# Optimization experiments

Measured on AMD Instinct MI355X. Metric: run time of the kernel, lower is better.

## Reference

```python
import jax, jax.numpy as jnp
import numpy as np

EMBED = 1024
HEADS = 16
HEAD_DIM = EMBED // HEADS


def setup_inputs() -> dict:
    key = jax.random.key(0)
    ks = jax.random.split(key, 12)
    B, S = 2, 2048
    inp = {
        'v': jax.random.normal(ks[0], (B, S, EMBED), jnp.float32),
        'k': jax.random.normal(ks[1], (B, S, EMBED), jnp.float32),
        'q': jax.random.normal(ks[2], (B, S, EMBED), jnp.float32),
        'mask': jnp.ones((B, 1, S, S), dtype=bool),
        'Wv': jax.random.normal(ks[3], (EMBED, EMBED), jnp.float32) * 0.02,
        'bv': jax.random.normal(ks[4], (EMBED,), jnp.float32) * 0.02,
        'Wk': jax.random.normal(ks[5], (EMBED, EMBED), jnp.float32) * 0.02,
        'bk': jax.random.normal(ks[6], (EMBED,), jnp.float32) * 0.02,
        'Wq': jax.random.normal(ks[7], (EMBED, EMBED), jnp.float32) * 0.02,
        'bq': jax.random.normal(ks[8], (EMBED,), jnp.float32) * 0.02,
        'Wo': jax.random.normal(ks[9], (EMBED, EMBED), jnp.float32) * 0.02,
        'bo': jax.random.normal(ks[10], (EMBED,), jnp.float32) * 0.02,
    }
    return inp


def reference(v, k, q, mask, Wv, bv, Wk, bk, Wq, bq, Wo, bo):
    N, q_len, _ = q.shape
    k_len = k.shape[1]
    # linear projections (torch Linear: x @ W.T + b)
    vh = (v @ Wv.T + bv).reshape(N, -1, HEADS, HEAD_DIM)
    kh = (k @ Wk.T + bk).reshape(N, k_len, HEADS, HEAD_DIM)
    qh = (q @ Wq.T + bq).reshape(N, q_len, HEADS, HEAD_DIM)
    # scores [N, H, q, k]
    energy = jnp.einsum('nqhd,nkhd->nhqk', qh, kh)
    # NOTE: original masks BEFORE dividing by sqrt(embed_size)
    energy = jnp.where(mask, energy, jnp.float32(-1e20))
    attention = jax.nn.softmax(energy / jnp.sqrt(jnp.float32(EMBED)), axis=3)
    out = jnp.einsum('nhqk,nkhd->nqhd', attention, vh).reshape(N, q_len, EMBED)
    return out @ Wo.T + bo
```

## Files before the change

kernel.cpp:

```cpp
#include <hip/hip_runtime.h>
#include <cstdint>
#include <cstddef>


typedef uint16_t u16;
typedef uint32_t u32;
typedef unsigned long long u64;
using bf16x8 = __attribute__((ext_vector_type(8))) __bf16;
using bf16x2 = __attribute__((ext_vector_type(2))) __bf16;
using f32x4  = __attribute__((ext_vector_type(4))) float;
using f32x16 = __attribute__((ext_vector_type(16))) float;
using u16x8  = __attribute__((ext_vector_type(8))) uint16_t;
using u16x4  = __attribute__((ext_vector_type(4))) uint16_t;
using u32x4  = __attribute__((ext_vector_type(4))) uint32_t;

#define S_LEN 2048
#define EMB   1024
#define NHEAD 16
#define HDIM  64
#define BATCH 2
#define MROWS (BATCH * S_LEN)
#define NBITW (BATCH * S_LEN * (S_LEN / 64))

__device__ __forceinline__ u16 f2bf(float f) {
  uint32_t u = __float_as_uint(f);
  u += 0x7FFFu + ((u >> 16) & 1u);
  return (u16)(u >> 16);
}

__device__ __forceinline__ float fexp2(float x) {
#if __has_builtin(__builtin_amdgcn_exp2f)
  return __builtin_amdgcn_exp2f(x);
#else
  return exp2f(x);
#endif
}

__device__ __forceinline__ u32 packbf(float a, float b) {
  bf16x2 v = { (__bf16)a, (__bf16)b };
  return __builtin_bit_cast(u32, v);
}

__device__ __forceinline__ void plswap(u32& a, u32& b) {
  asm volatile("v_permlane32_swap_b32 %0, %1" : "+v"(a), "+v"(b));
}

__device__ __forceinline__ float xhalf_sum(float x) {
  u32 a = __builtin_bit_cast(u32, x), b;
  asm volatile("v_mov_b32 %0, %1" : "=v"(b) : "v"(a));
  asm volatile("v_permlane32_swap_b32 %0, %1" : "+v"(a), "+v"(b));
  return __builtin_bit_cast(float, a) + __builtin_bit_cast(float, b);
}

__device__ __forceinline__ float tree16(const f32x16& v) {
  float t0 = v[0] + v[1], t1 = v[2] + v[3], t2 = v[4] + v[5], t3 = v[6] + v[7];
  float t4 = v[8] + v[9], t5 = v[10] + v[11], t6 = v[12] + v[13], t7 = v[14] + v[15];
  float u0 = t0 + t1, u1 = t2 + t3, u2 = t4 + t5, u3 = t6 + t7;
  return (u0 + u1) + (u2 + u3);
}

__device__ __forceinline__ void async16(void* lds, const void* g) {
  __builtin_amdgcn_global_load_lds(
      (const __attribute__((address_space(1))) void*)g,
      (__attribute__((address_space(3))) void*)lds, 16, 0, 0);
}

__global__ __launch_bounds__(256) void mask_compact(const uint32_t* __restrict__ m,
                                                    u64* __restrict__ bits) {
  const int i = blockIdx.x * 256 + threadIdx.x;
  if (i >= NBITW) return;
  const bool bytew = (m[0] == 0x01010101u);
  u64 b = 0;
  if (bytew) {
    const uint32_t* src = m + (size_t)i * 16;
#pragma unroll
    for (int w = 0; w < 16; ++w) {
      const uint32_t v = src[w];
#pragma unroll
      for (int j = 0; j < 4; ++j)
        b |= (u64)(((v >> (8 * j)) & 0xFFu) != 0u) << (w * 4 + j);
    }
  } else {
    const uint32_t* src = m + (size_t)i * 64;
#pragma unroll
    for (int j = 0; j < 64; ++j) b |= (u64)(src[j] != 0u) << j;
  }
  bits[i] = b;
}

struct ConvArgs {
  const float* src[4];
  u16* dst[4];
};

__global__ __launch_bounds__(256) void convert_bf16(ConvArgs a) {
  const int j = blockIdx.y;
  const float4* s = (const float4*)a.src[j];
  u16* d = a.dst[j];
  const int n4 = EMB * EMB / 4;
  for (int i = blockIdx.x * 256 + threadIdx.x; i < n4; i += gridDim.x * 256) {
    float4 v = s[i];
    u16x4 o = { f2bf(v.x), f2bf(v.y), f2bf(v.z), f2bf(v.w) };
    *(u16x4*)(d + (size_t)i * 4) = o;
  }
}

__device__ __forceinline__ void gemm_fused_body(const float* __restrict__ A,
                                                const u16* __restrict__ W,
                                                const float* __restrict__ bias,
                                                u16* __restrict__ C, float scale) {
  constexpr int K = 1024, N = 1024;
  __shared__ alignas(16) u16 As[128 * 32];
  __shared__ alignas(16) u16 Bs[128 * 32];
  const int t = threadIdx.x;
  const int wave = t >> 6, lane = t & 63;
  const int wr = wave >> 1, wc = wave & 1;
  const int m0 = blockIdx.y * 128, n0 = blockIdx.x * 128;
  f32x4 acc[4][4] = {};
  const int srow = wave * 16 + (lane >> 2);
  const int soff = (lane & 3) * 8;
  const u16* gB = W + (size_t)(n0 + srow) * K + soff;
  u16* lB = Bs + wave * 512;
  const int ar = t >> 1, ah = t & 1;
  const float* ga = A + (size_t)(m0 + ar) * K + ah * 16;
  u16* aw = As + ar * 32 + ah * 16;
  const int fo = (lane >> 4) * 8;
  const int fr = lane & 15;

  float4 v0 = *(const float4*)(ga + 0);
  float4 v1 = *(const float4*)(ga + 4);
  float4 v2 = *(const float4*)(ga + 8);
  float4 v3 = *(const float4*)(ga + 12);

  for (int kt = 0; kt < K; kt += 32) {
    {
      u16x8 w0 = { f2bf(v0.x), f2bf(v0.y), f2bf(v0.z), f2bf(v0.w),
                   f2bf(v1.x), f2bf(v1.y), f2bf(v1.z), f2bf(v1.w) };
      u16x8 w1 = { f2bf(v2.x), f2bf(v2.y), f2bf(v2.z), f2bf(v2.w),
                   f2bf(v3.x), f2bf(v3.y), f2bf(v3.z), f2bf(v3.w) };
      *(u16x8*)aw = w0;
      *(u16x8*)(aw + 8) = w1;
    }
    async16(lB,        gB + kt);
    async16(lB + 2048, gB + (size_t)64 * K + kt);
    __syncthreads();
    bf16x8 af[4], bfr[4];
#pragma unroll
    for (int i = 0; i < 4; ++i)
      af[i] = *(const bf16x8*)(As + (wr * 64 + i * 16 + fr) * 32 + fo);
#pragma unroll
    for (int i = 0; i < 4; ++i)
      bfr[i] = *(const bf16x8*)(Bs + (wc * 64 + i * 16 + fr) * 32 + fo);
#pragma unroll
    for (int mi = 0; mi < 4; ++mi)
#pragma unroll
      for (int ni = 0; ni < 4; ++ni)
        acc[mi][ni] = __builtin_amdgcn_mfma_f32_16x16x32_bf16(af[mi], bfr[ni],
                                                              acc[mi][ni], 0, 0, 0);
    if (kt + 32 < K) {
      v0 = *(const float4*)(ga + kt + 32);
      v1 = *(const float4*)(ga + kt + 36);
      v2 = *(const float4*)(ga + kt + 40);
      v3 = *(const float4*)(ga + kt + 44);
    }
    __syncthreads();
  }
  const int r0 = (lane >> 4) * 4;
#pragma unroll
  for (int mi = 0; mi < 4; ++mi) {
    const int rowb = m0 + wr * 64 + mi * 16 + r0;
#pragma unroll
    for (int ni = 0; ni < 4; ++ni) {
      const int col = n0 + wc * 64 + ni * 16 + fr;
      const float bv = bias[col];
#pragma unroll
      for (int r = 0; r < 4; ++r)
        C[(size_t)(rowb + r) * N + col] = f2bf((acc[mi][ni][r] + bv) * scale);
    }
  }
}

struct ProjArgs {
  const float* A[3];
  const u16* W[3];
  const float* bias[3];
  u16* C[3];
  float scale[3];
};

__global__ __launch_bounds__(256) void gemm_proj3(ProjArgs p) {
  const int z = blockIdx.z;
  gemm_fused_body(p.A[z], p.W[z], p.bias[z], p.C[z], p.scale[z]);
}

__global__ __launch_bounds__(256) void gemm_out(const u16* __restrict__ A,
                                                const u16* __restrict__ W,
                                                const float* __restrict__ bias,
                                                float* __restrict__ C) {
  constexpr int BM = 64, BN = 128, FM = 2, FN = 4;
  constexpr int K = 1024, N = 1024;
  __shared__ alignas(16) u16 As[BM * 32];
  __shared__ alignas(16) u16 Bs[BN * 32];
  const int t = threadIdx.x;
  const int wave = t >> 6, lane = t & 63;
  const int wr = wave >> 1, wc = wave & 1;
  const int m0 = blockIdx.y * BM, n0 = blockIdx.x * BN;
  f32x4 acc[FM][FN] = {};
  const int srow = wave * 16 + (lane >> 2);
  const int soff = (lane & 3) * 8;
  const u16* gA = A + (size_t)(m0 + srow) * K + soff;
  const u16* gB = W + (size_t)(n0 + srow) * K + soff;
  u16* lA = As + wave * 512;
  u16* lB = Bs + wave * 512;
  const int fo = (lane >> 4) * 8;
  const int fr = lane & 15;

  for (int kt = 0; kt < K; kt += 32) {
    async16(lA, gA + kt);
#pragma unroll
    for (int a = 0; a < BN / 64; ++a)
      async16(lB + a * 2048, gB + (size_t)(a * 64) * K + kt);
    __syncthreads();
    bf16x8 af[FM], bfr[FN];
#pragma unroll
    for (int i = 0; i < FM; ++i)
      af[i] = *(const bf16x8*)(As + (wr * (FM * 16) + i * 16 + fr) * 32 + fo);
#pragma unroll
    for (int i = 0; i < FN; ++i)
      bfr[i] = *(const bf16x8*)(Bs + (wc * (FN * 16) + i * 16 + fr) * 32 + fo);
#pragma unroll
    for (int mi = 0; mi < FM; ++mi)
#pragma unroll
      for (int ni = 0; ni < FN; ++ni)
        acc[mi][ni] = __builtin_amdgcn_mfma_f32_16x16x32_bf16(af[mi], bfr[ni],
                                                              acc[mi][ni], 0, 0, 0);
    __syncthreads();
  }
  const int r0 = (lane >> 4) * 4;
#pragma unroll
  for (int mi = 0; mi < FM; ++mi) {
    const int rowb = m0 + wr * (FM * 16) + mi * 16 + r0;
#pragma unroll
    for (int ni = 0; ni < FN; ++ni) {
      const int col = n0 + wc * (FN * 16) + ni * 16 + fr;
      const float bv = bias[col];
#pragma unroll
      for (int r = 0; r < 4; ++r)
        C[(size_t)(rowb + r) * N + col] = acc[mi][ni][r] + bv;
    }
  }
}

__global__ __launch_bounds__(256, 2) void attn_fa(const u16* __restrict__ Qh,
                                                  const u16* __restrict__ Kh,
                                                  const u16* __restrict__ Vh,
                                                  const u64* __restrict__ mbits,
                                                  u16* __restrict__ O) {
  __shared__ alignas(16) u16 Kt[2][64 * 64];
  __shared__ alignas(16) u16 Vt[2][64 * 64];
  const int t = threadIdx.x, wave = t >> 6, lane = t & 63;
  const int lin = blockIdx.x + 16 * blockIdx.y;
  const int logical = (lin & 7) * 64 + (lin >> 3);
  const int wbx = logical & 15;
  const int wbh = logical >> 4;
  const int b = wbh >> 4, h = wbh & 15;
  const int ql = lane & 31;
  const int hi = lane >> 5;
  const int qrow = wbx * 128 + wave * 32 + ql;

  const u16* qbase = Qh + (size_t)(b * S_LEN + qrow) * EMB + h * HDIM + hi * 8;
  bf16x8 qf[4];
#pragma unroll
  for (int dk = 0; dk < 4; ++dk)
    qf[dk] = *(const bf16x8*)(qbase + dk * 16);

  const int srow = t >> 3;
  const int schunk = t & 7;
  const int fk0 = (srow + (srow >> 3)) & 7;
  const int fk1 = (srow + 32 + ((srow + 32) >> 3)) & 7;
  const u16* kbase = Kh + (size_t)(b * S_LEN) * EMB + h * HDIM;
  const u16* vbase = Vh + (size_t)(b * S_LEN) * EMB + h * HDIM;
  const int vdg = t & 7, vkp = t >> 3;
  const int vd0 = vdg * 8, vk0 = vkp * 2;
  const int vg_hi = (vkp >> 2) & 7, vg_lo = (vkp & 3) * 4;

  u16x8 va, vb;
  {
    async16(&Kt[0][0] + wave * 512,
            kbase + (size_t)srow * EMB + ((schunk ^ fk0) * 8));
    async16(&Kt[0][0] + 2048 + wave * 512,
            kbase + (size_t)(srow + 32) * EMB + ((schunk ^ fk1) * 8));
    const u16* vs = vbase + (size_t)vk0 * EMB + vd0;
    va = *(const u16x8*)vs;
    vb = *(const u16x8*)(vs + EMB);
  }
#pragma unroll
  for (int j = 0; j < 8; ++j) {
    const int d = vd0 + j;
    const int fd = (d + (d >> 3)) & 7;
    const u32 val = (u32)va[j] | ((u32)vb[j] << 16);
    *(u32*)((char*)&Vt[0][0] + (d * 128 + ((vg_hi ^ fd) << 4) + vg_lo)) = val;
  }
  __syncthreads();

  f32x16 o[2] = {};
  float lloc = 0.f;
  const u64* mword = mbits + (size_t)(b * S_LEN + qrow) * 32;

  for (int kt = 0; kt < 32; ++kt) {
    const int cur = kt & 1, nxt = cur ^ 1;
    if (kt < 31) {
      const int kvn = (kt + 1) * 64;
      async16(&Kt[nxt][0] + wave * 512,
              kbase + (size_t)(kvn + srow) * EMB + ((schunk ^ fk0) * 8));
      async16(&Kt[nxt][0] + 2048 + wave * 512,
              kbase + (size_t)(kvn + srow + 32) * EMB + ((schunk ^ fk1) * 8));
      const u16* vs = vbase + (size_t)(kvn + vk0) * EMB + vd0;
      va = *(const u16x8*)vs;
      vb = *(const u16x8*)(vs + EMB);
    }

    f32x16 s[2] = {};
    __builtin_amdgcn_s_setprio(1);
#pragma unroll
    for (int kb = 0; kb < 2; ++kb) {
      const int key = kb * 32 + ql;
      const int fkk = (key + (key >> 3)) & 7;
      const char* kRow = (const char*)&Kt[cur][0] + key * 128;
#pragma unroll
      for (int dk = 0; dk < 4; ++dk) {
        const bf16x8 kf =
            *(const bf16x8*)(kRow + (((dk * 2 + hi) ^ fkk) << 4));
        s[kb] = __builtin_amdgcn_mfma_f32_32x32x16_bf16(kf, qf[dk], s[kb], 0, 0, 0);
      }
    }
    __builtin_amdgcn_s_setprio(0);

    const u64 mw = mword[kt];
    if (!__all((int)(mw == ~0ull))) {
#pragma unroll
      for (int kb = 0; kb < 2; ++kb)
#pragma unroll
        for (int r = 0; r < 16; ++r) {
          const int key = 32 * kb + (r & 3) + 8 * (r >> 2) + 4 * hi;
          if (!((mw >> key) & 1ull)) s[kb][r] = -1.0e20f;
        }
    }

#pragma unroll
    for (int kb = 0; kb < 2; ++kb)
#pragma unroll
      for (int r = 0; r < 16; ++r) s[kb][r] = fexp2(s[kb][r]);
    lloc += tree16(s[0]) + tree16(s[1]);

    bf16x8 pf[4];
#pragma unroll
    for (int kb = 0; kb < 2; ++kb) {
      u32 w0 = packbf(s[kb][0], s[kb][1]);
      u32 w1 = packbf(s[kb][2], s[kb][3]);
      u32 w2 = packbf(s[kb][4], s[kb][5]);
      u32 w3 = packbf(s[kb][6], s[kb][7]);
      u32 w4 = packbf(s[kb][8], s[kb][9]);
      u32 w5 = packbf(s[kb][10], s[kb][11]);
      u32 w6 = packbf(s[kb][12], s[kb][13]);
      u32 w7 = packbf(s[kb][14], s[kb][15]);
      plswap(w0, w2);
      plswap(w1, w3);
      plswap(w4, w6);
      plswap(w5, w7);
      const u32x4 lo4 = {w0, w1, w2, w3};
      const u32x4 hi4 = {w4, w5, w6, w7};
      pf[kb * 2 + 0] = __builtin_bit_cast(bf16x8, lo4);
      pf[kb * 2 + 1] = __builtin_bit_cast(bf16x8, hi4);
    }

    __builtin_amdgcn_s_setprio(1);
#pragma unroll
    for (int dB = 0; dB < 2; ++dB) {
      const int d = dB * 32 + ql;
      const int fd = (d + (d >> 3)) & 7;
      const char* vRow = (const char*)&Vt[cur][0] + d * 128;
#pragma unroll
      for (int ks = 0; ks < 4; ++ks) {
        const bf16x8 vf =
            *(const bf16x8*)(vRow + (((ks * 2 + hi) ^ fd) << 4));
        o[dB] = __builtin_amdgcn_mfma_f32_32x32x16_bf16(vf, pf[ks], o[dB], 0, 0, 0);
      }
    }
    __builtin_amdgcn_s_setprio(0);

    if (kt < 31) {
#pragma unroll
      for (int j = 0; j < 8; ++j) {
        const int d = vd0 + j;
        const int fd = (d + (d >> 3)) & 7;
        const u32 val = (u32)va[j] | ((u32)vb[j] << 16);
        *(u32*)((char*)&Vt[nxt][0] + (d * 128 + ((vg_hi ^ fd) << 4) + vg_lo)) = val;
      }
    }
    __syncthreads();
  }

  const float inv = 1.0f / xhalf_sum(lloc);
  u16* ob = O + (size_t)(b * S_LEN + qrow) * EMB + h * HDIM;
#pragma unroll
  for (int dB = 0; dB < 2; ++dB)
#pragma unroll
    for (int rr = 0; rr < 4; ++rr) {
      u16x4 st;
#pragma unroll
      for (int m = 0; m < 4; ++m) st[m] = f2bf(o[dB][rr * 4 + m] * inv);
      *(u16x4*)(ob + dB * 32 + rr * 8 + hi * 4) = st;
    }
}

extern "C" void kernel_launch(void* const* d_in, const int* in_sizes, int n_in,
                              void* d_out, int out_size, void* d_ws, size_t ws_size,
                              hipStream_t stream) {
  const float* v_in = (const float*)d_in[0];
  const float* k_in = (const float*)d_in[1];
  const float* q_in = (const float*)d_in[2];
  const uint32_t* mask = (const uint32_t*)d_in[3];
  const float* Wv = (const float*)d_in[4];
  const float* bv = (const float*)d_in[5];
  const float* Wk = (const float*)d_in[6];
  const float* bk = (const float*)d_in[7];
  const float* Wq = (const float*)d_in[8];
  const float* bq = (const float*)d_in[9];
  const float* Wo = (const float*)d_in[10];
  const float* bo = (const float*)d_in[11];

  char* ws = (char*)d_ws;
  const size_t SZX = (size_t)MROWS * EMB * 2;
  const size_t SZW = (size_t)EMB * EMB * 2;
  u16* qh  = (u16*)(ws);
  u16* kh  = (u16*)(ws + SZX);
  u16* vh  = (u16*)(ws + 2 * SZX);
  u16* Obf = (u16*)(ws + 3 * SZX);
  u16* Wqb = (u16*)(ws + 4 * SZX);
  u16* Wkb = (u16*)(ws + 4 * SZX + SZW);
  u16* Wvb = (u16*)(ws + 4 * SZX + 2 * SZW);
  u16* Wob = (u16*)(ws + 4 * SZX + 3 * SZW);
  u64* mbits = (u64*)(ws + 4 * SZX + 4 * SZW);

  mask_compact<<<dim3(NBITW / 256), 256, 0, stream>>>(mask, mbits);

  ConvArgs ca;
  ca.src[0] = Wq; ca.dst[0] = Wqb;
  ca.src[1] = Wk; ca.dst[1] = Wkb;
  ca.src[2] = Wv; ca.dst[2] = Wvb;
  ca.src[3] = Wo; ca.dst[3] = Wob;
  convert_bf16<<<dim3(128, 4), 256, 0, stream>>>(ca);

  ProjArgs pa;
  const float qscale = 1.4426950408889634f / 32.0f;
  pa.A[0] = q_in; pa.W[0] = Wqb; pa.bias[0] = bq; pa.C[0] = qh; pa.scale[0] = qscale;
  pa.A[1] = k_in; pa.W[1] = Wkb; pa.bias[1] = bk; pa.C[1] = kh; pa.scale[1] = 1.0f;
  pa.A[2] = v_in; pa.W[2] = Wvb; pa.bias[2] = bv; pa.C[2] = vh; pa.scale[2] = 1.0f;
  gemm_proj3<<<dim3(8, 32, 3), 256, 0, stream>>>(pa);

  attn_fa<<<dim3(16, 32), 256, 0, stream>>>(qh, kh, vh, mbits, Obf);

  gemm_out<<<dim3(8, 64), 256, 0, stream>>>(Obf, Wob, bo, (float*)d_out);
}
```

Baseline: 150.2 us.

## Pre-convert activations to bf16, use BK=64 swizzled async GEMM, remap block order

Q, K and V activations are now converted to bf16 in the shared conversion kernel, together with the weights. This lets the projection GEMM load both operands with async global-to-LDS copies instead of converting fp32 to bf16 inside the main loop. The projection K-tile doubles to 64 and uses an XOR-swizzled LDS layout to avoid bank conflicts. Block indices in the projection and output GEMMs are remapped so that blocks running at the same time share tiles in L2. The cost is an extra full write and read of bf16 activations, plus more workspace memory.

```diff
diff --git a/kernel.cpp b/kernel.cpp
--- a/kernel.cpp
+++ b/kernel.cpp
@@ -89,15 +89,16 @@
 }
 
 struct ConvArgs {
-  const float* src[4];
-  u16* dst[4];
+  const float* src[7];
+  u16* dst[7];
+  int n4[7];
 };
 
 __global__ __launch_bounds__(256) void convert_bf16(ConvArgs a) {
   const int j = blockIdx.y;
   const float4* s = (const float4*)a.src[j];
   u16* d = a.dst[j];
-  const int n4 = EMB * EMB / 4;
+  const int n4 = a.n4[j];
   for (int i = blockIdx.x * 256 + threadIdx.x; i < n4; i += gridDim.x * 256) {
     float4 v = s[i];
     u16x4 o = { f2bf(v.x), f2bf(v.y), f2bf(v.z), f2bf(v.w) };
@@ -105,63 +106,55 @@
   }
 }
 
-__device__ __forceinline__ void gemm_fused_body(const float* __restrict__ A,
-                                                const u16* __restrict__ W,
-                                                const float* __restrict__ bias,
-                                                u16* __restrict__ C, float scale) {
+__device__ __forceinline__ void gemm_body_bk64(const u16* __restrict__ A,
+                                               const u16* __restrict__ W,
+                                               const float* __restrict__ bias,
+                                               u16* __restrict__ C, float scale,
+                                               int m0, int n0) {
   constexpr int K = 1024, N = 1024;
-  __shared__ alignas(16) u16 As[128 * 32];
-  __shared__ alignas(16) u16 Bs[128 * 32];
+  __shared__ alignas(16) u16 As[128 * 64];
+  __shared__ alignas(16) u16 Bs[128 * 64];
   const int t = threadIdx.x;
   const int wave = t >> 6, lane = t & 63;
   const int wr = wave >> 1, wc = wave & 1;
-  const int m0 = blockIdx.y * 128, n0 = blockIdx.x * 128;
   f32x4 acc[4][4] = {};
-  const int srow = wave * 16 + (lane >> 2);
-  const int soff = (lane & 3) * 8;
-  const u16* gB = W + (size_t)(n0 + srow) * K + soff;
-  u16* lB = Bs + wave * 512;
-  const int ar = t >> 1, ah = t & 1;
-  const float* ga = A + (size_t)(m0 + ar) * K + ah * 16;
-  u16* aw = As + ar * 32 + ah * 16;
-  const int fo = (lane >> 4) * 8;
+  const int f = lane >> 3;
+  const int soff = ((lane & 7) ^ f) * 8;
+  const int srowp = wave * 8 + f;
   const int fr = lane & 15;
-
-  float4 v0 = *(const float4*)(ga + 0);
-  float4 v1 = *(const float4*)(ga + 4);
-  float4 v2 = *(const float4*)(ga + 8);
-  float4 v3 = *(const float4*)(ga + 12);
-
-  for (int kt = 0; kt < K; kt += 32) {
-    {
-      u16x8 w0 = { f2bf(v0.x), f2bf(v0.y), f2bf(v0.z), f2bf(v0.w),
-                   f2bf(v1.x), f2bf(v1.y), f2bf(v1.z), f2bf(v1.w) };
-      u16x8 w1 = { f2bf(v2.x), f2bf(v2.y), f2bf(v2.z), f2bf(v2.w),
-                   f2bf(v3.x), f2bf(v3.y), f2bf(v3.z), f2bf(v3.w) };
-      *(u16x8*)aw = w0;
-      *(u16x8*)(aw + 8) = w1;
-    }
-    async16(lB,        gB + kt);
-    async16(lB + 2048, gB + (size_t)64 * K + kt);
+  const int q4 = lane >> 4;
+
+  for (int kt = 0; kt < K; kt += 64) {
+#pragma unroll
+    for (int i = 0; i < 4; ++i)
+      async16(As + i * 2048 + wave * 512,
+              A + (size_t)(m0 + i * 32 + srowp) * K + kt + soff);
+#pragma unroll
+    for (int i = 0; i < 4; ++i)
+      async16(Bs + i * 2048 + wave * 512,
+              W + (size_t)(n0 + i * 32 + srowp) * K + kt + soff);
     __syncthreads();
-    bf16x8 af[4], bfr[4];
-#pragma unroll
-    for (int i = 0; i < 4; ++i)
-      af[i] = *(const bf16x8*)(As + (wr * 64 + i * 16 + fr) * 32 + fo);
-#pragma unroll
-    for (int i = 0; i < 4; ++i)
-      bfr[i] = *(const bf16x8*)(Bs + (wc * 64 + i * 16 + fr) * 32 + fo);
-#pragma unroll
-    for (int mi = 0; mi < 4; ++mi)
-#pragma unroll
-      for (int ni = 0; ni < 4; ++ni)
-        acc[mi][ni] = __builtin_amdgcn_mfma_f32_16x16x32_bf16(af[mi], bfr[ni],
-                                                              acc[mi][ni], 0, 0, 0);
-    if (kt + 32 < K) {
-      v0 = *(const float4*)(ga + kt + 32);
-      v1 = *(const float4*)(ga + kt + 36);
-      v2 = *(const float4*)(ga + kt + 40);
-      v3 = *(const float4*)(ga + kt + 44);
+#pragma unroll
+    for (int kk = 0; kk < 2; ++kk) {
+      bf16x8 af[4], bfr[4];
+#pragma unroll
+      for (int i = 0; i < 4; ++i) {
+        const int row = wr * 64 + i * 16 + fr;
+        af[i] = *(const bf16x8*)((const char*)As + row * 128 +
+                                 (((q4 + kk * 4) ^ (row & 7)) << 4));
+      }
+#pragma unroll
+      for (int i = 0; i < 4; ++i) {
+        const int row = wc * 64 + i * 16 + fr;
+        bfr[i] = *(const bf16x8*)((const char*)Bs + row * 128 +
+                                  (((q4 + kk * 4) ^ (row & 7)) << 4));
+      }
+#pragma unroll
+      for (int mi = 0; mi < 4; ++mi)
+#pragma unroll
+        for (int ni = 0; ni < 4; ++ni)
+          acc[mi][ni] = __builtin_amdgcn_mfma_f32_16x16x32_bf16(
+              af[mi], bfr[ni], acc[mi][ni], 0, 0, 0);
     }
     __syncthreads();
   }
@@ -181,7 +174,7 @@
 }
 
 struct ProjArgs {
-  const float* A[3];
+  const u16* A[3];
   const u16* W[3];
   const float* bias[3];
   u16* C[3];
@@ -189,8 +182,12 @@
 };
 
 __global__ __launch_bounds__(256) void gemm_proj3(ProjArgs p) {
-  const int z = blockIdx.z;
-  gemm_fused_body(p.A[z], p.W[z], p.bias[z], p.C[z], p.scale[z]);
+  const int lin = blockIdx.x + 8 * blockIdx.y + 256 * blockIdx.z;
+  const int logical = (lin & 7) * 96 + (lin >> 3);
+  const int z = logical >> 8;
+  const int rem = logical & 255;
+  const int n0 = (rem & 7) * 128, m0 = (rem >> 3) * 128;
+  gemm_body_bk64(p.A[z], p.W[z], p.bias[z], p.C[z], p.scale[z], m0, n0);
 }
 
 __global__ __launch_bounds__(256) void gemm_out(const u16* __restrict__ A,
@@ -204,7 +201,9 @@
   const int t = threadIdx.x;
   const int wave = t >> 6, lane = t & 63;
   const int wr = wave >> 1, wc = wave & 1;
-  const int m0 = blockIdx.y * BM, n0 = blockIdx.x * BN;
+  const int lin = blockIdx.x + 8 * blockIdx.y;
+  const int logical = (lin & 7) * 64 + (lin >> 3);
+  const int m0 = (logical >> 3) * BM, n0 = (logical & 7) * BN;
   f32x4 acc[FM][FN] = {};
   const int srow = wave * 16 + (lane >> 2);
   const int soff = (lane & 3) * 8;
@@ -441,22 +440,28 @@
   u16* Wkb = (u16*)(ws + 4 * SZX + SZW);
   u16* Wvb = (u16*)(ws + 4 * SZX + 2 * SZW);
   u16* Wob = (u16*)(ws + 4 * SZX + 3 * SZW);
-  u64* mbits = (u64*)(ws + 4 * SZX + 4 * SZW);
+  u16* qbf = (u16*)(ws + 4 * SZX + 4 * SZW);
+  u16* kbf = (u16*)(ws + 5 * SZX + 4 * SZW);
+  u16* vbf = (u16*)(ws + 6 * SZX + 4 * SZW);
+  u64* mbits = (u64*)(ws + 7 * SZX + 4 * SZW);
 
   mask_compact<<<dim3(NBITW / 256), 256, 0, stream>>>(mask, mbits);
 
   ConvArgs ca;
-  ca.src[0] = Wq; ca.dst[0] = Wqb;
-  ca.src[1] = Wk; ca.dst[1] = Wkb;
-  ca.src[2] = Wv; ca.dst[2] = Wvb;
-  ca.src[3] = Wo; ca.dst[3] = Wob;
-  convert_bf16<<<dim3(128, 4), 256, 0, stream>>>(ca);
+  ca.src[0] = q_in; ca.dst[0] = qbf; ca.n4[0] = MROWS * EMB / 4;
+  ca.src[1] = k_in; ca.dst[1] = kbf; ca.n4[1] = MROWS * EMB / 4;
+  ca.src[2] = v_in; ca.dst[2] = vbf; ca.n4[2] = MROWS * EMB / 4;
+  ca.src[3] = Wq;   ca.dst[3] = Wqb; ca.n4[3] = EMB * EMB / 4;
+  ca.src[4] = Wk;   ca.dst[4] = Wkb; ca.n4[4] = EMB * EMB / 4;
+  ca.src[5] = Wv;   ca.dst[5] = Wvb; ca.n4[5] = EMB * EMB / 4;
+  ca.src[6] = Wo;   ca.dst[6] = Wob; ca.n4[6] = EMB * EMB / 4;
+  convert_bf16<<<dim3(256, 7), 256, 0, stream>>>(ca);
 
   ProjArgs pa;
   const float qscale = 1.4426950408889634f / 32.0f;
-  pa.A[0] = q_in; pa.W[0] = Wqb; pa.bias[0] = bq; pa.C[0] = qh; pa.scale[0] = qscale;
-  pa.A[1] = k_in; pa.W[1] = Wkb; pa.bias[1] = bk; pa.C[1] = kh; pa.scale[1] = 1.0f;
-  pa.A[2] = v_in; pa.W[2] = Wvb; pa.bias[2] = bv; pa.C[2] = vh; pa.scale[2] = 1.0f;
+  pa.A[0] = qbf; pa.W[0] = Wqb; pa.bias[0] = bq; pa.C[0] = qh; pa.scale[0] = qscale;
+  pa.A[1] = kbf; pa.W[1] = Wkb; pa.bias[1] = bk; pa.C[1] = kh; pa.scale[1] = 1.0f;
+  pa.A[2] = vbf; pa.W[2] = Wvb; pa.bias[2] = bv; pa.C[2] = vh; pa.scale[2] = 1.0f;
   gemm_proj3<<<dim3(8, 32, 3), 256, 0, stream>>>(pa);
 
   attn_fa<<<dim3(16, 32), 256, 0, stream>>>(qh, kh, vh, mbits, Obf);
```

After: 133.8 us. 10.9% less time.
